# Performance work log

Measured on AMD Instinct MI355X. Metric: run time of the kernel, lower is better.

Reference implementation:

```python
import jax, jax.numpy as jnp
import numpy as np

NUM_GRIDS = 32
INPUT_DIM = 32
HIDDEN_DIM = 64
OUTPUT_DIM = 32
BATCH = 4096
INIT_SCALE = 0.1


def _borders_np(n_chunks):
    def inv_cdf(x):
        return np.log(2.0 * x) if x <= 0.5 else -np.log(2.0 * (1.0 - x))
    cs = 1.0 / n_chunks
    b = [inv_cdf(i * cs) for i in range(1, n_chunks)]
    left = b[0] - (b[1] - b[0])
    right = b[-1] + (b[-1] - b[-2])
    return np.array([left] + b + [right], dtype=np.float32)


def setup_inputs() -> dict:
    key = jax.random.key(0)
    k1, k2, k3 = jax.random.split(key, 3)
    Pi, Ph = INPUT_DIM // 2, HIDDEN_DIM // 2
    s0 = INIT_SCALE / np.sqrt(INPUT_DIM)
    s1 = INIT_SCALE / np.sqrt(INPUT_DIM * HIDDEN_DIM / 4)
    x = jax.random.normal(k1, (INPUT_DIM, BATCH), dtype=jnp.float32)
    level0_params = jax.random.uniform(k2, (NUM_GRIDS + 1, NUM_GRIDS + 1, HIDDEN_DIM, Pi),
                                       dtype=jnp.float32, minval=-s0, maxval=s0)
    level1_params = jax.random.uniform(k3, (NUM_GRIDS + 1, NUM_GRIDS + 1, OUTPUT_DIM, Pi, Ph),
                                       dtype=jnp.float32, minval=-s1, maxval=s1)
    b_np = _borders_np(NUM_GRIDS)
    borders = jnp.asarray(b_np)
    inv_chunk_lengths = jnp.asarray(1.0 / (b_np[1:] - b_np[:-1]))
    return {"x": x, "level0_params": level0_params, "level1_params": level1_params,
            "borders": borders, "inv_chunk_lengths": inv_chunk_lengths}


def _laplace_cdf(x):
    e = jnp.exp(-jnp.abs(x))
    return jnp.where(x > 0, 1.0 - 0.5 * e, 0.5 * e)


def _bilinear_interp(x1, x2, borders, inv_len, g):
    # x1, x2: [n_pairs, B]
    s1 = _laplace_cdf(x1) * g
    s2 = _laplace_cdf(x2) * g
    i1 = jnp.clip(s1.astype(jnp.int32), 0, g - 1)
    i2 = jnp.clip(s2.astype(jnp.int32), 0, g - 1)
    d1 = (x1 - borders[i1]) * inv_len[i1]
    d2 = (x2 - borders[i2]) * inv_len[i2]
    i1n = jnp.clip(i1 + 1, 0, g)
    i2n = jnp.clip(i2 + 1, 0, g)
    w00 = (1 - d1) * (1 - d2)
    w01 = (1 - d1) * d2
    w10 = d1 * (1 - d2)
    w11 = d1 * d2
    return i1, i2, i1n, i2n, w00, w01, w10, w11


def reference(x, level0_params, level1_params, borders, inv_chunk_lengths):
    g = NUM_GRIDS
    input_dim, B = x.shape
    Pi = input_dim // 2
    H = level0_params.shape[2]
    Ph = H // 2

    xp = x.reshape(Pi, 2, B)
    i1, i2, i1n, i2n, w00, w01, w10, w11 = _bilinear_interp(
        xp[:, 0], xp[:, 1], borders, inv_chunk_lengths, g)

    # level 0: gather 4 corners per (pair, batch) and weighted-accumulate -> z0 [H, B]
    l0t = jnp.transpose(level0_params, (3, 0, 1, 2))  # [Pi, g+1, g+1, H]
    pa = jnp.arange(Pi)[:, None]
    g00 = l0t[pa, i1, i2]    # [Pi, B, H]
    g01 = l0t[pa, i1, i2n]
    g10 = l0t[pa, i1n, i2]
    g11 = l0t[pa, i1n, i2n]
    z0 = (jnp.einsum('pb,pbh->hb', w00, g00)
          + jnp.einsum('pb,pbh->hb', w01, g01)
          + jnp.einsum('pb,pbh->hb', w10, g10)
          + jnp.einsum('pb,pbh->hb', w11, g11))

    z0p = z0.reshape(Ph, 2, B)
    j1, j2, j1n, j2n, wz00, wz01, wz10, wz11 = _bilinear_interp(
        z0p[:, 0], z0p[:, 1], borders, inv_chunk_lengths, g)

    # exactly as the torch loop (note: only idx1 of x and idxz1 of z are used).
    l1t = jnp.transpose(level1_params, (3, 4, 0, 1, 2))  # [Pi, Ph, g+1, g+1, O]
    xa = jnp.arange(Pi)[:, None, None]
    za = jnp.arange(Ph)[None, :, None]
    I1, I1n = i1[:, None, :], i1n[:, None, :]   # [Pi, 1, B]
    J1, J1n = j1[None, :, :], j1n[None, :, :]   # [1, Ph, B]
    q00 = l1t[xa, za, I1, J1]     # [Pi, Ph, B, O]
    q01 = l1t[xa, za, I1, J1n]
    q10 = l1t[xa, za, I1n, J1]
    q11 = l1t[xa, za, I1n, J1n]
    W00 = w00[:, None, :] * wz00[None, :, :]    # [Pi, Ph, B]
    W01 = w00[:, None, :] * wz10[None, :, :]
    W10 = w10[:, None, :] * wz00[None, :, :]
    W11 = w10[:, None, :] * wz10[None, :, :]
    out = (jnp.einsum('xzb,xzbo->ob', W00, q00)
           + jnp.einsum('xzb,xzbo->ob', W01, q01)
           + jnp.einsum('xzb,xzbo->ob', W10, q10)
           + jnp.einsum('xzb,xzbo->ob', W11, q11))
    return out
```

## Files before the change

kernel.cpp:

```cpp
#include <hip/hip_runtime.h>
#include <hip/hip_fp16.h>

#define NG 32
#define BATCH 4096

static constexpr size_t T1H_BYTES = 17842176ull * 2;
static constexpr size_t T0F_BYTES = 1115136ull * 4;

__device__ __forceinline__ void interp1(float v, const float* sb, const float* sil,
                                        int& i, float& d) {
    float e = expf(-fabsf(v));
    float s = (v > 0.f) ? (1.f - 0.5f * e) : (0.5f * e);
    s *= (float)NG;
    int ii = (int)s;
    ii = ii < 0 ? 0 : (ii > NG - 1 ? NG - 1 : ii);
    d = (v - sb[ii]) * sil[ii];
    i = ii;
}

__global__ __launch_bounds__(256) void k_transpose(
    const float* __restrict__ L1, const float* __restrict__ L0,
    __half* __restrict__ T1, float* __restrict__ T0)
{
    __shared__ __half hbuf[32 * 516];
    __shared__ float  fbuf[64 * 17];
    const int cell = blockIdx.x;
    const int tid = threadIdx.x;

    const float4* L1v = reinterpret_cast<const float4*>(L1 + (size_t)cell * 16384);
#pragma unroll
    for (int k = 0; k < 16; ++k) {
        int v = tid + k * 256;
        int idx = v * 4;
        int o = idx >> 9, r = idx & 511;
        float4 f = L1v[v];
        *reinterpret_cast<__half2*>(&hbuf[o * 516 + r])     = __float22half2_rn(make_float2(f.x, f.y));
        *reinterpret_cast<__half2*>(&hbuf[o * 516 + r + 2]) = __float22half2_rn(make_float2(f.z, f.w));
    }
    const float* L0s = L0 + (size_t)cell * 1024;
#pragma unroll
    for (int k = 0; k < 4; ++k) {
        int t = tid + k * 256;
        int h = t >> 4, p = t & 15;
        fbuf[h * 17 + p] = L0s[t];
    }
    __syncthreads();

#pragma unroll
    for (int k = 0; k < 8; ++k) {
        int t = tid + k * 256;
        int xz = t >> 2, o0 = (t & 3) * 8;
        __half tmp[8];
#pragma unroll
        for (int j = 0; j < 8; ++j) tmp[j] = hbuf[(o0 + j) * 516 + xz];
        *reinterpret_cast<uint4*>(&T1[((size_t)xz * 1089 + cell) * 32 + o0]) =
            *reinterpret_cast<const uint4*>(tmp);
    }
#pragma unroll
    for (int k = 0; k < 4; ++k) {
        int t = tid + k * 256;
        int p = t >> 6, h = t & 63;
        T0[((size_t)p * 1089 + cell) * 64 + h] = fbuf[h * 17 + p];
    }
}

__device__ __forceinline__ void accumh2(__half2 acc[4], uint4 u, __half2 c) {
    union { unsigned u32; __half2 h2; } cv;
    cv.u32 = u.x; acc[0] = __hfma2(c, cv.h2, acc[0]);
    cv.u32 = u.y; acc[1] = __hfma2(c, cv.h2, acc[1]);
    cv.u32 = u.z; acc[2] = __hfma2(c, cv.h2, acc[2]);
    cv.u32 = u.w; acc[3] = __hfma2(c, cv.h2, acc[3]);
}

__global__ __launch_bounds__(256, 4) void k_fused(
    const float* __restrict__ X, const float* __restrict__ T0,
    const __half* __restrict__ T1,
    const float* __restrict__ borders, const float* __restrict__ invlen,
    float* __restrict__ out)
{
    __shared__ float sb[33], sil[32];
    __shared__ int   scell[16][4];
    __shared__ float ssw[4][16][4];
    __shared__ float sz0[4][64];
    __shared__ int   si1[16][4];
    __shared__ float sX0[16][4], sX1[16][4];
    __shared__ int   sj1[32][4];
    __shared__ float sZ[2][32][4];

    const int tid = threadIdx.x;
    const int b0 = blockIdx.x * 4;

    if (tid < 33) sb[tid] = borders[tid];
    if (tid >= 64 && tid < 96) sil[tid - 64] = invlen[tid - 64];
    __syncthreads();

    if (tid < 64) {
        const int p = tid & 15, bl = tid >> 4;
        const int b = b0 + bl;
        float x1 = X[(2 * p) * BATCH + b];
        float x2 = X[(2 * p + 1) * BATCH + b];
        int i1, i2; float d1, d2;
        interp1(x1, sb, sil, i1, d1);
        interp1(x2, sb, sil, i2, d2);
        float w00 = (1.f - d1) * (1.f - d2);
        float w01 = (1.f - d1) * d2;
        float w10 = d1 * (1.f - d2);
        float w11 = d1 * d2;
        scell[p][bl] = i1 * 33 + i2;
        ssw[0][p][bl] = w00; ssw[1][p][bl] = w01; ssw[2][p][bl] = w10; ssw[3][p][bl] = w11;
        si1[p][bl] = i1;
        sX0[p][bl] = w00;
        sX1[p][bl] = w10;
    }
    __syncthreads();

    {
        const int h = tid & 63, bl = tid >> 6;
        float acc = 0.f;
#pragma unroll 4
        for (int p = 0; p < 16; ++p) {
            int cell = scell[p][bl];
            unsigned basep = ((unsigned)p * 1089u + (unsigned)cell) * 64u + (unsigned)h;
            float t00 = T0[basep];
            float t01 = T0[basep + 64];
            float t10 = T0[basep + 33 * 64];
            float t11 = T0[basep + 34 * 64];
            acc += ssw[0][p][bl] * t00 + ssw[1][p][bl] * t01 + ssw[2][p][bl] * t10 + ssw[3][p][bl] * t11;
        }
        sz0[bl][h] = acc;
    }
    __syncthreads();

    if (tid < 128) {
        const int z = tid & 31, bl = tid >> 5;
        float z1 = sz0[bl][2 * z];
        float z2 = sz0[bl][2 * z + 1];
        int j1, j2u; float dz1, dz2;
        interp1(z1, sb, sil, j1, dz1);
        interp1(z2, sb, sil, j2u, dz2);
        (void)j2u;
        sj1[z][bl] = j1;
        sZ[0][z][bl] = (1.f - dz1) * (1.f - dz2);
        sZ[1][z][bl] = dz1 * (1.f - dz2);
    }
    __syncthreads();

    const int lane = tid & 63, bl = tid >> 6;
    const int b = b0 + bl;
    const int oh = lane & 3;
    const int jc = (lane >> 2) & 1;
    const int zs = lane >> 3;
    const unsigned loff = (unsigned)(jc * 32 + oh * 8);

    __half2 acc2[4];
#pragma unroll
    for (int k = 0; k < 4; ++k) acc2[k] = __half2half2(__float2half(0.f));

#pragma unroll 2
    for (int x = 0; x < 16; ++x) {
        const int cb = si1[x][bl] * 33;
        const float X0 = sX0[x][bl], X1 = sX1[x][bl];
        const unsigned xzb = (unsigned)(x * 32 + zs * 4) * 1089u;
#pragma unroll
        for (int zi = 0; zi < 4; ++zi) {
            const int z = zs * 4 + zi;
            const unsigned cell = (unsigned)(cb + sj1[z][bl]);
            const float Zc = sZ[jc][z][bl];
            const unsigned base = (xzb + (unsigned)zi * 1089u + cell) * 32u + loff;
            uint4 u0 = *reinterpret_cast<const uint4*>(T1 + base);
            uint4 u1 = *reinterpret_cast<const uint4*>(T1 + base + 33 * 32);
            const float c0 = X0 * Zc, c1 = X1 * Zc;
            accumh2(acc2, u0, __float2half2_rn(c0));
            accumh2(acc2, u1, __float2half2_rn(c1));
        }
    }

    float accf[8];
#pragma unroll
    for (int k = 0; k < 4; ++k) {
        float2 f = __half22float2(acc2[k]);
        accf[2 * k] = f.x; accf[2 * k + 1] = f.y;
    }
#pragma unroll
    for (int m = 4; m <= 32; m <<= 1) {
#pragma unroll
        for (int k = 0; k < 8; ++k) accf[k] += __shfl_xor(accf[k], m, 64);
    }
    if (lane < 4) {
#pragma unroll
        for (int k = 0; k < 8; ++k) out[(oh * 8 + k) * BATCH + b] = accf[k];
    }
}

extern "C" void kernel_launch(void* const* d_in, const int* in_sizes, int n_in,
                              void* d_out, int out_size, void* d_ws, size_t ws_size,
                              hipStream_t stream) {
    const float* X       = (const float*)d_in[0];
    const float* L0      = (const float*)d_in[1];
    const float* L1      = (const float*)d_in[2];
    const float* borders = (const float*)d_in[3];
    const float* invlen  = (const float*)d_in[4];
    float* out = (float*)d_out;

    char* ws = (char*)d_ws;
    __half* T1h = (__half*)ws;
    float*  T0f = (float*)(ws + T1H_BYTES);

    hipLaunchKernelGGL(k_transpose, dim3(1089), dim3(256), 0, stream, L1, L0, T1h, T0f);
    hipLaunchKernelGGL(k_fused, dim3(BATCH / 4), dim3(256), 0, stream,
                       X, T0f, T1h, borders, invlen, out);
}
```

Before: 149.6 us.

## Split fused kernel into prep and x-split main kernel with atomic accumulation

```diff
diff --git a/kernel.cpp b/kernel.cpp
--- a/kernel.cpp
+++ b/kernel.cpp
@@ -64,34 +64,24 @@
     }
 }
 
-__device__ __forceinline__ void accumh2(__half2 acc[4], uint4 u, __half2 c) {
-    union { unsigned u32; __half2 h2; } cv;
-    cv.u32 = u.x; acc[0] = __hfma2(c, cv.h2, acc[0]);
-    cv.u32 = u.y; acc[1] = __hfma2(c, cv.h2, acc[1]);
-    cv.u32 = u.z; acc[2] = __hfma2(c, cv.h2, acc[2]);
-    cv.u32 = u.w; acc[3] = __hfma2(c, cv.h2, acc[3]);
-}
-
-__global__ __launch_bounds__(256, 4) void k_fused(
+__global__ __launch_bounds__(256) void k_prep(
     const float* __restrict__ X, const float* __restrict__ T0,
-    const __half* __restrict__ T1,
     const float* __restrict__ borders, const float* __restrict__ invlen,
+    int* __restrict__ i1x, float* __restrict__ wx0, float* __restrict__ wx1,
+    int* __restrict__ j1z, float* __restrict__ wz0, float* __restrict__ wz1,
     float* __restrict__ out)
 {
     __shared__ float sb[33], sil[32];
     __shared__ int   scell[16][4];
     __shared__ float ssw[4][16][4];
     __shared__ float sz0[4][64];
-    __shared__ int   si1[16][4];
-    __shared__ float sX0[16][4], sX1[16][4];
-    __shared__ int   sj1[32][4];
-    __shared__ float sZ[2][32][4];
 
     const int tid = threadIdx.x;
     const int b0 = blockIdx.x * 4;
 
     if (tid < 33) sb[tid] = borders[tid];
     if (tid >= 64 && tid < 96) sil[tid - 64] = invlen[tid - 64];
+    if (tid >= 128) out[blockIdx.x * 128 + (tid - 128)] = 0.f;
     __syncthreads();
 
     if (tid < 64) {
@@ -108,9 +98,9 @@
         float w11 = d1 * d2;
         scell[p][bl] = i1 * 33 + i2;
         ssw[0][p][bl] = w00; ssw[1][p][bl] = w01; ssw[2][p][bl] = w10; ssw[3][p][bl] = w11;
-        si1[p][bl] = i1;
-        sX0[p][bl] = w00;
-        sX1[p][bl] = w10;
+        i1x[p * BATCH + b] = i1;
+        wx0[p * BATCH + b] = w00;
+        wx1[p * BATCH + b] = w10;
     }
     __syncthreads();
 
@@ -133,15 +123,52 @@
 
     if (tid < 128) {
         const int z = tid & 31, bl = tid >> 5;
+        const int b = b0 + bl;
         float z1 = sz0[bl][2 * z];
         float z2 = sz0[bl][2 * z + 1];
         int j1, j2u; float dz1, dz2;
         interp1(z1, sb, sil, j1, dz1);
         interp1(z2, sb, sil, j2u, dz2);
         (void)j2u;
-        sj1[z][bl] = j1;
-        sZ[0][z][bl] = (1.f - dz1) * (1.f - dz2);
-        sZ[1][z][bl] = dz1 * (1.f - dz2);
+        j1z[z * BATCH + b] = j1;
+        wz0[z * BATCH + b] = (1.f - dz1) * (1.f - dz2);
+        wz1[z * BATCH + b] = dz1 * (1.f - dz2);
+    }
+}
+
+__device__ __forceinline__ void accumh2(__half2 acc[4], uint4 u, __half2 c) {
+    union { unsigned u32; __half2 h2; } cv;
+    cv.u32 = u.x; acc[0] = __hfma2(c, cv.h2, acc[0]);
+    cv.u32 = u.y; acc[1] = __hfma2(c, cv.h2, acc[1]);
+    cv.u32 = u.z; acc[2] = __hfma2(c, cv.h2, acc[2]);
+    cv.u32 = u.w; acc[3] = __hfma2(c, cv.h2, acc[3]);
+}
+
+__global__ __launch_bounds__(256, 4) void k_main(
+    const __half* __restrict__ T1,
+    const int* __restrict__ i1x, const float* __restrict__ wx0, const float* __restrict__ wx1,
+    const int* __restrict__ j1z, const float* __restrict__ wz0, const float* __restrict__ wz1,
+    float* __restrict__ out)
+{
+    __shared__ int   si1[2][4];
+    __shared__ float sX0[2][4], sX1[2][4];
+    __shared__ int   sj1[32][4];
+    __shared__ float sZ[2][32][4];
+
+    const int tid = threadIdx.x;
+    const int xg = blockIdx.x & 7;
+    const int b0 = (blockIdx.x >> 3) * 4;
+
+    if (tid < 8) {
+        int xi = tid >> 2, bl = tid & 3;
+        int x = xg * 2 + xi;
+        int idx = x * BATCH + b0 + bl;
+        si1[xi][bl] = i1x[idx]; sX0[xi][bl] = wx0[idx]; sX1[xi][bl] = wx1[idx];
+    }
+    if (tid < 128) {
+        int z = tid >> 2, bl = tid & 3;
+        int idx = z * BATCH + b0 + bl;
+        sj1[z][bl] = j1z[idx]; sZ[0][z][bl] = wz0[idx]; sZ[1][z][bl] = wz1[idx];
     }
     __syncthreads();
 
@@ -156,10 +183,11 @@
 #pragma unroll
     for (int k = 0; k < 4; ++k) acc2[k] = __half2half2(__float2half(0.f));
 
-#pragma unroll 2
-    for (int x = 0; x < 16; ++x) {
-        const int cb = si1[x][bl] * 33;
-        const float X0 = sX0[x][bl], X1 = sX1[x][bl];
+#pragma unroll
+    for (int xi = 0; xi < 2; ++xi) {
+        const int x = xg * 2 + xi;
+        const int cb = si1[xi][bl] * 33;
+        const float X0 = sX0[xi][bl], X1 = sX1[xi][bl];
         const unsigned xzb = (unsigned)(x * 32 + zs * 4) * 1089u;
 #pragma unroll
         for (int zi = 0; zi < 4; ++zi) {
@@ -188,7 +216,8 @@
     }
     if (lane < 4) {
 #pragma unroll
-        for (int k = 0; k < 8; ++k) out[(oh * 8 + k) * BATCH + b] = accf[k];
+        for (int k = 0; k < 8; ++k)
+            unsafeAtomicAdd(&out[(oh * 8 + k) * BATCH + b], accf[k]);
     }
 }
 
@@ -205,8 +234,17 @@
     char* ws = (char*)d_ws;
     __half* T1h = (__half*)ws;
     float*  T0f = (float*)(ws + T1H_BYTES);
+    char* p = ws + T1H_BYTES + T0F_BYTES;
+    int*   i1x = (int*)p;            p += 16 * BATCH * 4;
+    float* wx0 = (float*)p;          p += 16 * BATCH * 4;
+    float* wx1 = (float*)p;          p += 16 * BATCH * 4;
+    int*   j1z = (int*)p;            p += 32 * BATCH * 4;
+    float* wz0 = (float*)p;          p += 32 * BATCH * 4;
+    float* wz1 = (float*)p;          p += 32 * BATCH * 4;
 
     hipLaunchKernelGGL(k_transpose, dim3(1089), dim3(256), 0, stream, L1, L0, T1h, T0f);
-    hipLaunchKernelGGL(k_fused, dim3(BATCH / 4), dim3(256), 0, stream,
-                       X, T0f, T1h, borders, invlen, out);
-}
+    hipLaunchKernelGGL(k_prep, dim3(BATCH / 4), dim3(256), 0, stream,
+                       X, T0f, borders, invlen, i1x, wx0, wx1, j1z, wz0, wz1, out);
+    hipLaunchKernelGGL(k_main, dim3((BATCH / 4) * 8), dim3(256), 0, stream,
+                       T1h, i1x, wx0, wx1, j1z, wz0, wz1, out);
+}
```

Result: slower. 263.1 us (+75.9%).
